# Optimization experiments

Hardware: AMD Instinct MI355X
Metric: run time of the kernel (lower is better)

Reference implementation:

```python
import jax, jax.numpy as jnp
import numpy as np

NEG_SLOPE = 0.2  # PyG GATConv default LeakyReLU slope


def gat_conv(x, src, dst, W, a_src, a_dst, b):
    """Single-head GATConv (PyG defaults: heads=1, add_self_loops already done).
    x: [N, F_in]; src/dst: [E] int (self loops included); W: [F_in, F_out];
    a_src, a_dst: [F_out]; b: [F_out].
    """
    N = x.shape[0]
    h = x @ W                           # [N, F_out]
    alpha_src = h @ a_src               # [N]
    alpha_dst = h @ a_dst               # [N]
    e = alpha_src[src] + alpha_dst[dst]  # [E]
    e = jnp.where(e > 0, e, NEG_SLOPE * e)  # LeakyReLU
    # numerically stable segment softmax over edges grouped by dst
    m = jax.ops.segment_max(e, dst, num_segments=N)      # [N]
    ex = jnp.exp(e - m[dst])                             # [E]
    denom = jax.ops.segment_sum(ex, dst, num_segments=N)  # [N]
    alpha = ex / denom[dst]                              # [E]
    out = jax.ops.segment_sum(alpha[:, None] * h[src], dst, num_segments=N)
    return out + b


def add_self_loops(edge_index, N):
    loop = jnp.arange(N, dtype=edge_index.dtype)
    src = jnp.concatenate([edge_index[0], loop])
    dst = jnp.concatenate([edge_index[1], loop])
    return src, dst


def setup_inputs() -> dict:
    key = jax.random.key(0)
    N, E = 100000, 1600000
    dims = [128, 128, 128, 128]  # in -> hidden0 -> hidden1 -> out
    ks = jax.random.split(key, 16)
    inp = {
        "x": jax.random.normal(ks[0], (N, dims[0]), dtype=jnp.float32),
        "edge_index": jax.random.randint(ks[1], (2, E), 0, N, dtype=jnp.int32),
    }
    ki = 2
    for l in range(3):
        fi, fo = dims[l], dims[l + 1]
        inp[f"W{l}"] = jax.random.normal(ks[ki], (fi, fo), dtype=jnp.float32) * (1.0 / np.sqrt(fi)); ki += 1
        inp[f"a_src{l}"] = jax.random.normal(ks[ki], (fo,), dtype=jnp.float32) * 0.1; ki += 1
        inp[f"a_dst{l}"] = jax.random.normal(ks[ki], (fo,), dtype=jnp.float32) * 0.1; ki += 1
        inp[f"b{l}"] = jnp.zeros((fo,), dtype=jnp.float32); ki += 1
    return inp


def reference(x, edge_index,
              W0, a_src0, a_dst0, b0,
              W1, a_src1, a_dst1, b1,
              W2, a_src2, a_dst2, b2):
    N = x.shape[0]
    src, dst = add_self_loops(edge_index, N)
    h = gat_conv(x, src, dst, W0, a_src0, a_dst0, b0)
    h = jax.nn.elu(h)
    h = gat_conv(h, src, dst, W1, a_src1, a_dst1, b1)
    h = jax.nn.elu(h)
    out = gat_conv(h, src, dst, W2, a_src2, a_dst2, b2)
    return out
```

## Files before the change

### kernel.cpp

```cpp
#include <hip/hip_runtime.h>
#include <hip/hip_bf16.h>
#include <hip/hip_fp16.h>
#include <math.h>

#define NEG_SLOPE 0.2f

typedef unsigned int uint;
typedef __bf16 bf16x8 __attribute__((ext_vector_type(8)));
typedef __bf16 bf16x4 __attribute__((ext_vector_type(4)));
typedef __bf16 bf16x2 __attribute__((ext_vector_type(2)));
typedef _Float16 f16x2 __attribute__((ext_vector_type(2)));
typedef float floatx4 __attribute__((ext_vector_type(4)));

#define CPAD 5

__device__ inline float2 h2_to_f2(uint v) {
    f16x2 p = __builtin_bit_cast(f16x2, v);
    return make_float2((float)p[0], (float)p[1]);
}


__global__ void count_deg_rank(const int* __restrict__ dst, int* __restrict__ deg,
                               int* __restrict__ rank, int E) {
    int t = blockIdx.x * blockDim.x + threadIdx.x;
    int stride = gridDim.x * blockDim.x;
    int E4 = E >> 2;
    for (int i4 = t; i4 < E4; i4 += stride) {
        int4 d4 = ((const int4*)dst)[i4];
        int4 r4;
        r4.x = atomicAdd(&deg[d4.x << CPAD], 1);
        r4.y = atomicAdd(&deg[d4.y << CPAD], 1);
        r4.z = atomicAdd(&deg[d4.z << CPAD], 1);
        r4.w = atomicAdd(&deg[d4.w << CPAD], 1);
        ((int4*)rank)[i4] = r4;
    }
    for (int i = (E4 << 2) + t; i < E; i += stride)
        rank[i] = atomicAdd(&deg[dst[i] << CPAD], 1);
}

__global__ void scan_block_k(const int* __restrict__ deg, int* __restrict__ off,
                             int* __restrict__ bsum, int N) {
    __shared__ int sdata[256];
    int t = threadIdx.x;
    int base = blockIdx.x * 1024 + t * 4;
    int v0 = (base + 0 < N) ? deg[(base + 0) << CPAD] : 0;
    int v1 = (base + 1 < N) ? deg[(base + 1) << CPAD] : 0;
    int v2 = (base + 2 < N) ? deg[(base + 2) << CPAD] : 0;
    int v3 = (base + 3 < N) ? deg[(base + 3) << CPAD] : 0;
    int s = v0 + v1 + v2 + v3;
    sdata[t] = s;
    __syncthreads();
    for (int d = 1; d < 256; d <<= 1) {
        int x = (t >= d) ? sdata[t - d] : 0;
        __syncthreads();
        sdata[t] += x;
        __syncthreads();
    }
    int run = sdata[t] - s;
    if (t == 255) bsum[blockIdx.x] = sdata[255];
    if (base + 0 < N) off[base + 0] = run; run += v0;
    if (base + 1 < N) off[base + 1] = run; run += v1;
    if (base + 2 < N) off[base + 2] = run; run += v2;
    if (base + 3 < N) off[base + 3] = run;
}

__global__ void scan_bsum_k(int* bsum, int G) {
    __shared__ int sdata[1024];
    int t = threadIdx.x;
    int v = (t < G) ? bsum[t] : 0;
    sdata[t] = v;
    __syncthreads();
    for (int d = 1; d < 1024; d <<= 1) {
        int x = (t >= d) ? sdata[t - d] : 0;
        __syncthreads();
        sdata[t] += x;
        __syncthreads();
    }
    if (t < G) bsum[t] = sdata[t] - v;
}

__global__ void add_bsum_k(int* __restrict__ off, const int* __restrict__ bsum,
                           int N, int Etot) {
    int i = blockIdx.x * blockDim.x + threadIdx.x;
    if (i < N) off[i] += bsum[i >> 10];
    else if (i == N) off[N] = Etot;
}

__global__ void fill_scatter(const int* __restrict__ src, const int* __restrict__ dst,
                             const int* __restrict__ rank, const int* __restrict__ off,
                             int* __restrict__ csr_src, int E) {
    int t = blockIdx.x * blockDim.x + threadIdx.x;
    int stride = gridDim.x * blockDim.x;
    int E4 = E >> 2;
    for (int i4 = t; i4 < E4; i4 += stride) {
        int4 d4 = ((const int4*)dst)[i4];
        int4 s4 = ((const int4*)src)[i4];
        int4 r4 = ((const int4*)rank)[i4];
        csr_src[off[d4.x] + r4.x] = s4.x;
        csr_src[off[d4.y] + r4.y] = s4.y;
        csr_src[off[d4.z] + r4.z] = s4.z;
        csr_src[off[d4.w] + r4.w] = s4.w;
    }
    for (int i = (E4 << 2) + t; i < E; i += stride)
        csr_src[off[dst[i]] + rank[i]] = src[i];
}


__global__ void split_x_k(const float* __restrict__ in, __bf16* __restrict__ hi,
                          __bf16* __restrict__ lo, int n4) {
    int i = blockIdx.x * blockDim.x + threadIdx.x;
    if (i >= n4) return;
    float4 v = ((const float4*)in)[i];
    bf16x4 h = { (__bf16)v.x, (__bf16)v.y, (__bf16)v.z, (__bf16)v.w };
    bf16x4 l = { (__bf16)(v.x - (float)h[0]), (__bf16)(v.y - (float)h[1]),
                 (__bf16)(v.z - (float)h[2]), (__bf16)(v.w - (float)h[3]) };
    ((bf16x4*)hi)[i] = h;
    ((bf16x4*)lo)[i] = l;
}

__global__ void split_w_k(const float* __restrict__ W0, const float* __restrict__ W1,
                          const float* __restrict__ W2, __bf16* __restrict__ Wfh,
                          __bf16* __restrict__ Wfl) {
    const float* W = (blockIdx.y == 0) ? W0 : (blockIdx.y == 1) ? W1 : W2;
    size_t base = (size_t)blockIdx.y * 16384;
    int i = blockIdx.x * 256 + threadIdx.x;
    int k = i >> 7, ncol = i & 127;
    int ct = ncol >> 4, n16 = ncol & 15;
    int kt = k >> 5, q = (k & 31) >> 3, j = k & 7;
    size_t flat = (size_t)(((ct * 4 + kt) * 64) + q * 16 + n16) * 8 + j;
    float v = W[i];
    __bf16 h = (__bf16)v;
    __bf16 l = (__bf16)(v - (float)h);
    Wfh[base + flat] = h;
    Wfl[base + flat] = l;
}


__global__ __launch_bounds__(512, 2) void gemm_split(
    const __bf16* __restrict__ Ah, const __bf16* __restrict__ Al,
    const __bf16* __restrict__ Wh, const __bf16* __restrict__ Wl,
    const float* __restrict__ avs, const float* __restrict__ avd,
    _Float16* __restrict__ Hh, float* __restrict__ asrc, float* __restrict__ adst,
    int M) {
    __shared__ __align__(16) char lds_raw[65536];
    int tid = threadIdx.x;
    int wv = tid >> 6, lane = tid & 63;
    int n = lane & 15, q = lane >> 4;

    #pragma unroll
    for (int it = 0; it < 8; ++it) {
        int boff = it * 8192 + tid * 16;
        const char* s = (it < 4) ? ((const char*)Wh + boff)
                                 : ((const char*)Wl + (boff - 32768));
        *(float4*)(lds_raw + boff) = *(const float4*)s;
    }

    int arow_g = blockIdx.x * 128 + wv * 16 + n;
    int arow_c = (arow_g < M) ? arow_g : (M - 1);
    const bf16x8* ah = (const bf16x8*)(Ah + (size_t)arow_c * 128);
    const bf16x8* al = (const bf16x8*)(Al + (size_t)arow_c * 128);
    bf16x8 a_h[4], a_l[4];
    #pragma unroll
    for (int kt = 0; kt < 4; ++kt) {
        a_h[kt] = ah[kt * 4 + q];
        a_l[kt] = al[kt * 4 + q];
    }
    __syncthreads();

    floatx4 acc[8];
    #pragma unroll
    for (int ct = 0; ct < 8; ++ct) {
        floatx4 c = {0.f, 0.f, 0.f, 0.f};
        #pragma unroll
        for (int kt = 0; kt < 4; ++kt) {
            int fo = ((ct * 4 + kt) * 64 + lane) * 16;
            bf16x8 bh = *(const bf16x8*)(lds_raw + fo);
            bf16x8 bl = *(const bf16x8*)(lds_raw + 32768 + fo);
            c = __builtin_amdgcn_mfma_f32_16x16x32_bf16(a_h[kt], bh, c, 0, 0, 0);
            c = __builtin_amdgcn_mfma_f32_16x16x32_bf16(a_h[kt], bl, c, 0, 0, 0);
            c = __builtin_amdgcn_mfma_f32_16x16x32_bf16(a_l[kt], bh, c, 0, 0, 0);
        }
        acc[ct] = c;
    }

    float ps[4] = {0.f, 0.f, 0.f, 0.f}, pd[4] = {0.f, 0.f, 0.f, 0.f};
    #pragma unroll
    for (int ct = 0; ct < 8; ++ct) {
        float sv = avs[ct * 16 + n], dv = avd[ct * 16 + n];
        #pragma unroll
        for (int r = 0; r < 4; ++r) {
            ps[r] += acc[ct][r] * sv;
            pd[r] += acc[ct][r] * dv;
        }
    }
    #pragma unroll
    for (int m = 1; m < 16; m <<= 1) {
        #pragma unroll
        for (int r = 0; r < 4; ++r) {
            ps[r] += __shfl_xor(ps[r], m, 64);
            pd[r] += __shfl_xor(pd[r], m, 64);
        }
    }
    if (n == 0) {
        #pragma unroll
        for (int r = 0; r < 4; ++r) {
            int grow = blockIdx.x * 128 + wv * 16 + q * 4 + r;
            if (grow < M) { asrc[grow] = ps[r]; adst[grow] = pd[r]; }
        }
    }

    __syncthreads();
    _Float16 (*hl)[132] = (_Float16(*)[132])lds_raw;
    #pragma unroll
    for (int ct = 0; ct < 8; ++ct)
        #pragma unroll
        for (int r = 0; r < 4; ++r)
            hl[wv * 16 + q * 4 + r][ct * 16 + n] = (_Float16)acc[ct][r];
    __syncthreads();

    int r0 = blockIdx.x * 128;
    for (int i = tid; i < 128 * 64; i += 512) {
        int rr = i >> 6, cu = i & 63;
        int gr = r0 + rr;
        if (gr < M)
            ((uint*)Hh)[(size_t)gr * 64 + cu] = *(const uint*)&hl[rr][cu * 2];
    }
}


#define EW_CAP 128

template <int FINAL>
__global__ __launch_bounds__(256) void aggregate_k(
    const _Float16* __restrict__ h, const float* __restrict__ asrc,
    const float* __restrict__ adst, const int* __restrict__ off,
    const int* __restrict__ csr, const float* __restrict__ bias,
    float* __restrict__ out_f, __bf16* __restrict__ a_hi, __bf16* __restrict__ a_lo,
    int N, int E) {
    __shared__ int2 srec[4][EW_CAP];
    int gid = blockIdx.x * blockDim.x + threadIdx.x;
    int wid = gid >> 6, lane = gid & 63;
    int wv = (threadIdx.x >> 6);
    if (wid >= N) return;
    const uint* hrows = (const uint*)h;
    float ad = adst[wid];
    float acc0, acc1, denom;

    {
        float e = asrc[wid] + ad;
        e = (e > 0.f) ? e : NEG_SLOPE * e;
        float w = __expf(e);
        float2 f = h2_to_f2(hrows[(size_t)wid * 64 + lane]);
        denom = w; acc0 = w * f.x; acc1 = w * f.y;
    }

    int beg = __builtin_amdgcn_readfirstlane(off[wid]);
    int end = __builtin_amdgcn_readfirstlane(off[wid + 1]);

    for (int sc = beg; sc < end; sc += EW_CAP) {
        int cnt = end - sc; cnt = (cnt < EW_CAP) ? cnt : EW_CAP;

        for (int e0 = lane; e0 < cnt; e0 += 64) {
            int s = csr[sc + e0];
            float e = asrc[s] + ad;
            e = (e > 0.f) ? e : NEG_SLOPE * e;
            srec[wv][e0] = make_int2(__float_as_int(__expf(e)), s);
        }
        asm volatile("s_waitcnt lgkmcnt(0)" ::: "memory");

        int cm1 = cnt - 1;
        for (int j = 0; j < cnt; j += 8) {
            int2 r0 = srec[wv][j];
            int2 r1 = srec[wv][(j + 1 <= cm1) ? j + 1 : cm1];
            int2 r2 = srec[wv][(j + 2 <= cm1) ? j + 2 : cm1];
            int2 r3 = srec[wv][(j + 3 <= cm1) ? j + 3 : cm1];
            int2 r4 = srec[wv][(j + 4 <= cm1) ? j + 4 : cm1];
            int2 r5 = srec[wv][(j + 5 <= cm1) ? j + 5 : cm1];
            int2 r6 = srec[wv][(j + 6 <= cm1) ? j + 6 : cm1];
            int2 r7 = srec[wv][(j + 7 <= cm1) ? j + 7 : cm1];
            int s0 = __builtin_amdgcn_readfirstlane(r0.y);
            int s1 = __builtin_amdgcn_readfirstlane(r1.y);
            int s2 = __builtin_amdgcn_readfirstlane(r2.y);
            int s3 = __builtin_amdgcn_readfirstlane(r3.y);
            int s4 = __builtin_amdgcn_readfirstlane(r4.y);
            int s5 = __builtin_amdgcn_readfirstlane(r5.y);
            int s6 = __builtin_amdgcn_readfirstlane(r6.y);
            int s7 = __builtin_amdgcn_readfirstlane(r7.y);
            uint v0 = hrows[(size_t)s0 * 64 + lane];
            uint v1 = hrows[(size_t)s1 * 64 + lane];
            uint v2 = hrows[(size_t)s2 * 64 + lane];
            uint v3 = hrows[(size_t)s3 * 64 + lane];
            uint v4 = hrows[(size_t)s4 * 64 + lane];
            uint v5 = hrows[(size_t)s5 * 64 + lane];
            uint v6 = hrows[(size_t)s6 * 64 + lane];
            uint v7 = hrows[(size_t)s7 * 64 + lane];

            float w0 = __int_as_float(r0.x);
            float w1 = (j + 1 < cnt) ? __int_as_float(r1.x) : 0.f;
            float w2 = (j + 2 < cnt) ? __int_as_float(r2.x) : 0.f;
            float w3 = (j + 3 < cnt) ? __int_as_float(r3.x) : 0.f;
            float w4 = (j + 4 < cnt) ? __int_as_float(r4.x) : 0.f;
            float w5 = (j + 5 < cnt) ? __int_as_float(r5.x) : 0.f;
            float w6 = (j + 6 < cnt) ? __int_as_float(r6.x) : 0.f;
            float w7 = (j + 7 < cnt) ? __int_as_float(r7.x) : 0.f;

            denom += (w0 + w1) + (w2 + w3);
            float2 f0 = h2_to_f2(v0), f1 = h2_to_f2(v1);
            float2 f2 = h2_to_f2(v2), f3 = h2_to_f2(v3);
            acc0 += w0 * f0.x + w1 * f1.x + w2 * f2.x + w3 * f3.x;
            acc1 += w0 * f0.y + w1 * f1.y + w2 * f2.y + w3 * f3.y;

            denom += (w4 + w5) + (w6 + w7);
            float2 f4 = h2_to_f2(v4), f5 = h2_to_f2(v5);
            float2 f6 = h2_to_f2(v6), f7 = h2_to_f2(v7);
            acc0 += w4 * f4.x + w5 * f5.x + w6 * f6.x + w7 * f7.x;
            acc1 += w4 * f4.y + w5 * f5.y + w6 * f6.y + w7 * f7.y;
        }
        asm volatile("s_waitcnt lgkmcnt(0)" ::: "memory");
    }

    float inv = 1.0f / denom;
    float2 b2 = ((const float2*)bias)[lane];
    float o0 = acc0 * inv + b2.x;
    float o1 = acc1 * inv + b2.y;
    if (FINAL) {
        ((float2*)out_f)[(size_t)wid * 64 + lane] = make_float2(o0, o1);
    } else {
        o0 = (o0 > 0.f) ? o0 : (__expf(o0) - 1.0f);
        o1 = (o1 > 0.f) ? o1 : (__expf(o1) - 1.0f);
        __bf16 h0 = (__bf16)o0, h1 = (__bf16)o1;
        bf16x2 ph = { h0, h1 };
        bf16x2 pl = { (__bf16)(o0 - (float)h0), (__bf16)(o1 - (float)h1) };
        ((bf16x2*)a_hi)[(size_t)wid * 64 + lane] = ph;
        ((bf16x2*)a_lo)[(size_t)wid * 64 + lane] = pl;
    }
}


extern "C" void kernel_launch(void* const* d_in, const int* in_sizes, int n_in,
                              void* d_out, int out_size, void* d_ws, size_t ws_size,
                              hipStream_t stream) {
    const float* x = (const float*)d_in[0];
    const int* ei = (const int*)d_in[1];
    int N = in_sizes[0] / 128;
    int E = in_sizes[1] / 2;
    const int* src = ei;
    const int* dst = ei + E;

    const float* Wl_[3] = { (const float*)d_in[2], (const float*)d_in[6], (const float*)d_in[10] };
    const float* asl[3] = { (const float*)d_in[3], (const float*)d_in[7], (const float*)d_in[11] };
    const float* adl[3] = { (const float*)d_in[4], (const float*)d_in[8], (const float*)d_in[12] };
    const float* bl[3]  = { (const float*)d_in[5], (const float*)d_in[9], (const float*)d_in[13] };

    size_t nfeat = (size_t)N * 128;
    char* p = (char*)d_ws;
    _Float16* Hh = (_Float16*)p; p += nfeat * 2;
    __bf16* Wfh = (__bf16*)p; p += 3 * 16384 * 2;
    __bf16* Wfl = (__bf16*)p; p += 3 * 16384 * 2;
    float* asrc = (float*)p;  p += (size_t)N * 4;
    float* adst = (float*)p;  p += (size_t)N * 4;
    int* off    = (int*)p;    p += (size_t)(N + 1) * 4;
    int* bsum   = (int*)p;    p += 4096 * 4;
    int* csr    = (int*)p;    p += (size_t)E * 4;

    int* cpad = (int*)Hh;
    int* rank = (int*)((char*)Hh + ((size_t)N << CPAD) * sizeof(int));

    __bf16* A_hi = (__bf16*)d_out;
    __bf16* A_lo = A_hi + nfeat;

    int G = (N + 1023) / 1024;

    hipMemsetAsync(cpad, 0, ((size_t)N << CPAD) * sizeof(int), stream);
    count_deg_rank<<<2048, 256, 0, stream>>>(dst, cpad, rank, E);
    scan_block_k<<<G, 256, 0, stream>>>(cpad, off, bsum, N);
    scan_bsum_k<<<1, 1024, 0, stream>>>(bsum, G);
    add_bsum_k<<<(N + 256) / 256, 256, 0, stream>>>(off, bsum, N, E);
    fill_scatter<<<2048, 256, 0, stream>>>(src, dst, rank, off, csr, E);

    split_w_k<<<dim3(64, 3), 256, 0, stream>>>(Wl_[0], Wl_[1], Wl_[2], Wfh, Wfl);
    int n4 = (int)(nfeat / 4);
    split_x_k<<<(n4 + 255) / 256, 256, 0, stream>>>(x, A_hi, A_lo, n4);

    int gemm_blocks = (N + 127) / 128;
    int wave_blocks = (N + 3) / 4;

    for (int l = 0; l < 3; ++l) {
        gemm_split<<<gemm_blocks, 512, 0, stream>>>(
            A_hi, A_lo, Wfh + (size_t)l * 16384, Wfl + (size_t)l * 16384,
            asl[l], adl[l], Hh, asrc, adst, N);
        if (l < 2) {
            aggregate_k<0><<<wave_blocks, 256, 0, stream>>>(
                Hh, asrc, adst, off, csr, bl[l], nullptr, A_hi, A_lo, N, E);
        } else {
            aggregate_k<1><<<wave_blocks, 256, 0, stream>>>(
                Hh, asrc, adst, off, csr, bl[l], (float*)d_out, nullptr, nullptr, N, E);
        }
    }
}
```

Measured before the change: 504.7 us.

## Fuse preprocessing kernels and overlap CSR fill with first GEMM

Merges degree counting/ranking, weight splitting and input bf16 hi/lo splitting into one heterogeneous prep kernel. Appends extra blocks to the first-layer GEMM launch that perform the CSR scatter fill, so the fill runs concurrently with the GEMM instead of as a separate launch. Rank moves to its own workspace buffer, since Hh is now written while rank is still being read. This reduces launch count and serialization, at the cost of extra workspace and extra parameters and a branch in the GEMM kernel.

Result: no change. 511.1 us (+1.3%).

```diff
diff --git a/kernel.cpp b/kernel.cpp
--- a/kernel.cpp
+++ b/kernel.cpp
@@ -13,6 +13,8 @@
 typedef float floatx4 __attribute__((ext_vector_type(4)));
 
 #define CPAD 5
+#define CNT_BLKS 2048
+#define FILL_BLKS 1024
 
 __device__ inline float2 h2_to_f2(uint v) {
     f16x2 p = __builtin_bit_cast(f16x2, v);
@@ -20,23 +22,56 @@
 }
 
 
-__global__ void count_deg_rank(const int* __restrict__ dst, int* __restrict__ deg,
-                               int* __restrict__ rank, int E) {
-    int t = blockIdx.x * blockDim.x + threadIdx.x;
-    int stride = gridDim.x * blockDim.x;
-    int E4 = E >> 2;
-    for (int i4 = t; i4 < E4; i4 += stride) {
-        int4 d4 = ((const int4*)dst)[i4];
-        int4 r4;
-        r4.x = atomicAdd(&deg[d4.x << CPAD], 1);
-        r4.y = atomicAdd(&deg[d4.y << CPAD], 1);
-        r4.z = atomicAdd(&deg[d4.z << CPAD], 1);
-        r4.w = atomicAdd(&deg[d4.w << CPAD], 1);
-        ((int4*)rank)[i4] = r4;
-    }
-    for (int i = (E4 << 2) + t; i < E; i += stride)
-        rank[i] = atomicAdd(&deg[dst[i] << CPAD], 1);
-}
+__global__ __launch_bounds__(256) void prep_k(
+    const int* __restrict__ dst, int* __restrict__ deg, int* __restrict__ rank,
+    int E,
+    const float* __restrict__ x, __bf16* __restrict__ xhi, __bf16* __restrict__ xlo,
+    int n4,
+    const float* __restrict__ W0, const float* __restrict__ W1,
+    const float* __restrict__ W2, __bf16* __restrict__ Wfh, __bf16* __restrict__ Wfl) {
+    int b = blockIdx.x, tid = threadIdx.x;
+    if (b < CNT_BLKS) {
+        int t = b * 256 + tid;
+        int stride = CNT_BLKS * 256;
+        int E4 = E >> 2;
+        for (int i4 = t; i4 < E4; i4 += stride) {
+            int4 d4 = ((const int4*)dst)[i4];
+            int4 r4;
+            r4.x = atomicAdd(&deg[d4.x << CPAD], 1);
+            r4.y = atomicAdd(&deg[d4.y << CPAD], 1);
+            r4.z = atomicAdd(&deg[d4.z << CPAD], 1);
+            r4.w = atomicAdd(&deg[d4.w << CPAD], 1);
+            ((int4*)rank)[i4] = r4;
+        }
+        for (int i = (E4 << 2) + t; i < E; i += stride)
+            rank[i] = atomicAdd(&deg[dst[i] << CPAD], 1);
+    } else if (b < CNT_BLKS + 192) {
+        int wb = b - CNT_BLKS;
+        const float* W = (wb < 64) ? W0 : (wb < 128) ? W1 : W2;
+        size_t base = (size_t)(wb >> 6) * 16384;
+        int i = (wb & 63) * 256 + tid;
+        int k = i >> 7, ncol = i & 127;
+        int ct = ncol >> 4, n16 = ncol & 15;
+        int kt = k >> 5, q = (k & 31) >> 3, j = k & 7;
+        size_t flat = (size_t)(((ct * 4 + kt) * 64) + q * 16 + n16) * 8 + j;
+        float v = W[i];
+        __bf16 h = (__bf16)v;
+        __bf16 l = (__bf16)(v - (float)h);
+        Wfh[base + flat] = h;
+        Wfl[base + flat] = l;
+    } else {
+        int i = (b - CNT_BLKS - 192) * 256 + tid;
+        if (i < n4) {
+            float4 v = ((const float4*)x)[i];
+            bf16x4 h = { (__bf16)v.x, (__bf16)v.y, (__bf16)v.z, (__bf16)v.w };
+            bf16x4 l = { (__bf16)(v.x - (float)h[0]), (__bf16)(v.y - (float)h[1]),
+                         (__bf16)(v.z - (float)h[2]), (__bf16)(v.w - (float)h[3]) };
+            ((bf16x4*)xhi)[i] = h;
+            ((bf16x4*)xlo)[i] = l;
+        }
+    }
+}
+
 
 __global__ void scan_block_k(const int* __restrict__ deg, int* __restrict__ off,
                              int* __restrict__ bsum, int N) {
@@ -86,64 +121,37 @@
     else if (i == N) off[N] = Etot;
 }
 
-__global__ void fill_scatter(const int* __restrict__ src, const int* __restrict__ dst,
-                             const int* __restrict__ rank, const int* __restrict__ off,
-                             int* __restrict__ csr_src, int E) {
-    int t = blockIdx.x * blockDim.x + threadIdx.x;
-    int stride = gridDim.x * blockDim.x;
-    int E4 = E >> 2;
-    for (int i4 = t; i4 < E4; i4 += stride) {
-        int4 d4 = ((const int4*)dst)[i4];
-        int4 s4 = ((const int4*)src)[i4];
-        int4 r4 = ((const int4*)rank)[i4];
-        csr_src[off[d4.x] + r4.x] = s4.x;
-        csr_src[off[d4.y] + r4.y] = s4.y;
-        csr_src[off[d4.z] + r4.z] = s4.z;
-        csr_src[off[d4.w] + r4.w] = s4.w;
-    }
-    for (int i = (E4 << 2) + t; i < E; i += stride)
-        csr_src[off[dst[i]] + rank[i]] = src[i];
-}
-
-
-__global__ void split_x_k(const float* __restrict__ in, __bf16* __restrict__ hi,
-                          __bf16* __restrict__ lo, int n4) {
-    int i = blockIdx.x * blockDim.x + threadIdx.x;
-    if (i >= n4) return;
-    float4 v = ((const float4*)in)[i];
-    bf16x4 h = { (__bf16)v.x, (__bf16)v.y, (__bf16)v.z, (__bf16)v.w };
-    bf16x4 l = { (__bf16)(v.x - (float)h[0]), (__bf16)(v.y - (float)h[1]),
-                 (__bf16)(v.z - (float)h[2]), (__bf16)(v.w - (float)h[3]) };
-    ((bf16x4*)hi)[i] = h;
-    ((bf16x4*)lo)[i] = l;
-}
-
-__global__ void split_w_k(const float* __restrict__ W0, const float* __restrict__ W1,
-                          const float* __restrict__ W2, __bf16* __restrict__ Wfh,
-                          __bf16* __restrict__ Wfl) {
-    const float* W = (blockIdx.y == 0) ? W0 : (blockIdx.y == 1) ? W1 : W2;
-    size_t base = (size_t)blockIdx.y * 16384;
-    int i = blockIdx.x * 256 + threadIdx.x;
-    int k = i >> 7, ncol = i & 127;
-    int ct = ncol >> 4, n16 = ncol & 15;
-    int kt = k >> 5, q = (k & 31) >> 3, j = k & 7;
-    size_t flat = (size_t)(((ct * 4 + kt) * 64) + q * 16 + n16) * 8 + j;
-    float v = W[i];
-    __bf16 h = (__bf16)v;
-    __bf16 l = (__bf16)(v - (float)h);
-    Wfh[base + flat] = h;
-    Wfl[base + flat] = l;
-}
-
 
 __global__ __launch_bounds__(512, 2) void gemm_split(
     const __bf16* __restrict__ Ah, const __bf16* __restrict__ Al,
     const __bf16* __restrict__ Wh, const __bf16* __restrict__ Wl,
     const float* __restrict__ avs, const float* __restrict__ avd,
     _Float16* __restrict__ Hh, float* __restrict__ asrc, float* __restrict__ adst,
-    int M) {
+    int M,
+    const int* __restrict__ srcE, const int* __restrict__ dstE,
+    const int* __restrict__ rank, const int* __restrict__ off,
+    int* __restrict__ csr_src, int E, int gemmBlocks) {
     __shared__ __align__(16) char lds_raw[65536];
     int tid = threadIdx.x;
+
+    if ((int)blockIdx.x >= gemmBlocks) {
+        int t = ((int)blockIdx.x - gemmBlocks) * 512 + tid;
+        int stride = ((int)gridDim.x - gemmBlocks) * 512;
+        int E4 = E >> 2;
+        for (int i4 = t; i4 < E4; i4 += stride) {
+            int4 d4 = ((const int4*)dstE)[i4];
+            int4 s4 = ((const int4*)srcE)[i4];
+            int4 r4 = ((const int4*)rank)[i4];
+            csr_src[off[d4.x] + r4.x] = s4.x;
+            csr_src[off[d4.y] + r4.y] = s4.y;
+            csr_src[off[d4.z] + r4.z] = s4.z;
+            csr_src[off[d4.w] + r4.w] = s4.w;
+        }
+        for (int i = (E4 << 2) + t; i < E; i += stride)
+            csr_src[off[dstE[i]] + rank[i]] = srcE[i];
+        return;
+    }
+
     int wv = tid >> 6, lane = tid & 63;
     int n = lane & 15, q = lane >> 4;
 
@@ -362,33 +370,40 @@
     int* off    = (int*)p;    p += (size_t)(N + 1) * 4;
     int* bsum   = (int*)p;    p += 4096 * 4;
     int* csr    = (int*)p;    p += (size_t)E * 4;
+    int* rank   = (int*)p;    p += (size_t)E * 4;
 
     int* cpad = (int*)Hh;
-    int* rank = (int*)((char*)Hh + ((size_t)N << CPAD) * sizeof(int));
 
     __bf16* A_hi = (__bf16*)d_out;
     __bf16* A_lo = A_hi + nfeat;
 
     int G = (N + 1023) / 1024;
+    int n4 = (int)(nfeat / 4);
 
     hipMemsetAsync(cpad, 0, ((size_t)N << CPAD) * sizeof(int), stream);
-    count_deg_rank<<<2048, 256, 0, stream>>>(dst, cpad, rank, E);
+    int prep_blocks = CNT_BLKS + 192 + (n4 + 255) / 256;
+    prep_k<<<prep_blocks, 256, 0, stream>>>(
+        dst, cpad, rank, E, x, A_hi, A_lo, n4,
+        Wl_[0], Wl_[1], Wl_[2], Wfh, Wfl);
+
     scan_block_k<<<G, 256, 0, stream>>>(cpad, off, bsum, N);
     scan_bsum_k<<<1, 1024, 0, stream>>>(bsum, G);
     add_bsum_k<<<(N + 256) / 256, 256, 0, stream>>>(off, bsum, N, E);
-    fill_scatter<<<2048, 256, 0, stream>>>(src, dst, rank, off, csr, E);
-
-    split_w_k<<<dim3(64, 3), 256, 0, stream>>>(Wl_[0], Wl_[1], Wl_[2], Wfh, Wfl);
-    int n4 = (int)(nfeat / 4);
-    split_x_k<<<(n4 + 255) / 256, 256, 0, stream>>>(x, A_hi, A_lo, n4);
 
     int gemm_blocks = (N + 127) / 128;
     int wave_blocks = (N + 3) / 4;
 
     for (int l = 0; l < 3; ++l) {
-        gemm_split<<<gemm_blocks, 512, 0, stream>>>(
-            A_hi, A_lo, Wfh + (size_t)l * 16384, Wfl + (size_t)l * 16384,
-            asl[l], adl[l], Hh, asrc, adst, N);
+        if (l == 0) {
+            gemm_split<<<gemm_blocks + FILL_BLKS, 512, 0, stream>>>(
+                A_hi, A_lo, Wfh, Wfl, asl[0], adl[0], Hh, asrc, adst, N,
+                src, dst, rank, off, csr, E, gemm_blocks);
+        } else {
+            gemm_split<<<gemm_blocks, 512, 0, stream>>>(
+                A_hi, A_lo, Wfh + (size_t)l * 16384, Wfl + (size_t)l * 16384,
+                asl[l], adl[l], Hh, asrc, adst, N,
+                nullptr, nullptr, nullptr, nullptr, nullptr, 0, gemm_blocks);
+        }
         if (l < 2) {
             aggregate_k<0><<<wave_blocks, 256, 0, stream>>>(
                 Hh, asrc, adst, off, csr, bl[l], nullptr, A_hi, A_lo, N, E);
```
